# Optimization experiments

Hardware: AMD Instinct MI355X
Metric: run time of the kernel (lower is better)

The kernel has to match this reference:

```python
import jax, jax.numpy as jnp
import numpy as np

B, L, D, H, DF = 8, 1024, 512, 8, 2048
NBLK = 3  # three TemporalAttentionBlocks


def _ln(x, g, b, eps=1e-5):
    m = x.mean(-1, keepdims=True)
    v = x.var(-1, keepdims=True)
    return (x - m) / jnp.sqrt(v + eps) * g + b


def setup_inputs() -> dict:
    key = jax.random.key(0)
    ks = iter(jax.random.split(key, 64))
    def w(i, o):
        return jax.random.normal(next(ks), (i, o), jnp.float32) * (1.0 / np.sqrt(i))
    def ws(n, i, o):
        return jax.random.normal(next(ks), (n, i, o), jnp.float32) * (1.0 / np.sqrt(i))
    return dict(
        x=jax.random.normal(next(ks), (B, L, D), jnp.float32),
        # outer multi-head attention (AttentionLayer) params
        aw_q=w(D, D), ab_q=jnp.zeros((D,), jnp.float32),
        aw_k=w(D, D), ab_k=jnp.zeros((D,), jnp.float32),
        aw_v=w(D, D), ab_v=jnp.zeros((D,), jnp.float32),
        aw_o=w(D, D), ab_o=jnp.zeros((D,), jnp.float32),
        n1g=jnp.ones((D,), jnp.float32), n1b=jnp.zeros((D,), jnp.float32),
        n2g=jnp.ones((D,), jnp.float32), n2b=jnp.zeros((D,), jnp.float32),
        # 3 stacked TemporalAttentionBlock params
        tqw=ws(NBLK, D, D), tqb=jnp.zeros((NBLK, D), jnp.float32),
        tkw=ws(NBLK, D, D), tkb=jnp.zeros((NBLK, D), jnp.float32),
        tvw=ws(NBLK, D, D), tvb=jnp.zeros((NBLK, D), jnp.float32),
        tow=ws(NBLK, D, D), tob=jnp.zeros((NBLK, D), jnp.float32),
        tf1w=ws(NBLK, D, DF), tf1b=jnp.zeros((NBLK, DF), jnp.float32),
        tf2w=ws(NBLK, DF, D), tf2b=jnp.zeros((NBLK, D), jnp.float32),
        tng=jnp.ones((NBLK, D), jnp.float32), tnb=jnp.zeros((NBLK, D), jnp.float32),
    )


def _temporal_block(x, qw, qb, kw, kb, vw, vb, ow, ob, f1w, f1b, f2w, f2b, ng, nb):
    b, l, d = x.shape
    q = x @ qw + qb
    k = x @ kw + kb
    v = x @ vw + vb
    # NOTE: no 1/sqrt(d) scaling, as in the original
    probs = jax.nn.softmax(jnp.einsum('bld,bsd->bls', q, k), axis=-1)
    out = jnp.einsum('bls,bsd->bld', probs, v)
    # faithful to original transpose(1,2).contiguous().view(-1, L, D): a
    # memory-reinterpreting reshape of [B,D,L] into [B,L,D]
    out = jnp.swapaxes(out, 1, 2).reshape(b, l, d)
    x = x + (out @ ow + ob)
    res = x
    xn = _ln(x, ng, nb)
    ff = jax.nn.relu(xn @ f1w + f1b) @ f2w + f2b
    return res + ff


def reference(x, aw_q, ab_q, aw_k, ab_k, aw_v, ab_v, aw_o, ab_o,
              n1g, n1b, n2g, n2b,
              tqw, tqb, tkw, tkb, tvw, tvb, tow, tob,
              tf1w, tf1b, tf2w, tf2b, tng, tnb):
    b, l, d = x.shape
    e = d // H
    q = (x @ aw_q + ab_q).reshape(b, l, H, e)
    k = (x @ aw_k + ab_k).reshape(b, l, H, e)
    v = (x @ aw_v + ab_v).reshape(b, l, H, e)
    A = jax.nn.softmax(jnp.einsum('blhe,bshe->bhls', q, k) / np.sqrt(e).astype(np.float32), axis=-1)
    new_x = jnp.einsum('bhls,bshe->blhe', A, v).reshape(b, l, d) @ aw_o + ab_o
    x = _ln(x + new_x, n1g, n1b)
    y = x
    for i in range(NBLK):
        y = _temporal_block(y, tqw[i], tqb[i], tkw[i], tkb[i], tvw[i], tvb[i],
                            tow[i], tob[i], tf1w[i], tf1b[i], tf2w[i], tf2b[i],
                            tng[i], tnb[i])
    return _ln(x + y, n2g, n2b), A
```

## Files before the change

kernel.cpp:

```cpp
#include <hip/hip_runtime.h>

typedef __bf16 bf16;
typedef __bf16 v8bf __attribute__((ext_vector_type(8)));
typedef float  v4f  __attribute__((ext_vector_type(4)));

#define BM 128
#define BN 128
#define BK 32

enum { EPI_STORE = 0, EPI_RELU = 1, EPI_ADD = 2 };

template <int SPLIT, int EPI, typename CT>
__global__ __launch_bounds__(256)
void gemm_bt(const bf16* __restrict__ A, long plA,
             const bf16* __restrict__ Bt, long plB,
             const float* __restrict__ bias, long sBias,
             const bf16* __restrict__ R, long plR,
             CT* __restrict__ C, long plC,
             int M, int N, int K, int lda, int ldb, int ldc,
             long sA, long sB, long sC, long sR,
             int zdiv, long sA2, long sB2, long sC2,
             float scale)
{
    constexpr int NBUF = SPLIT ? 4 : 2;
    __shared__ __attribute__((aligned(16))) bf16 lds[NBUF * BM * BK];
    bf16* const lAh = lds;
    bf16* const lBh = lds + BM * BK;
    bf16* const lAl = SPLIT ? lds + 2 * BM * BK : lds;
    bf16* const lBl = SPLIT ? lds + 3 * BM * BK : lds;

    const int bz = blockIdx.z;
    const int zq = bz / zdiv;
    const int zr = bz - zq * zdiv;
    A  += (long)zq * sA + (long)zr * sA2;
    Bt += (long)zq * sB + (long)zr * sB2;
    C  += (long)zq * sC + (long)zr * sC2;
    const float* bp = bias ? bias + (long)bz * sBias : nullptr;
    const bf16* Rp = (EPI == EPI_ADD) ? (R + (long)zq * sR) : (const bf16*)nullptr;

    const int tn = blockIdx.x * BN;
    const int tm = blockIdx.y * BM;
    const int tid  = threadIdx.x;
    const int wave = tid >> 6;
    const int lane = tid & 63;
    const int wm   = (wave >> 1) * 64;
    const int wn   = (wave & 1) * 64;
    const int quad = lane >> 4;
    const int l16  = lane & 15;

    v4f acc[4][4];
#pragma unroll
    for (int i = 0; i < 4; ++i)
#pragma unroll
        for (int j = 0; j < 4; ++j) {
            v4f z = {0.f, 0.f, 0.f, 0.f};
            acc[i][j] = z;
        }

    const int sr  = lane >> 2;
    const int scl = (lane & 3) * 8;

    for (int k0 = 0; k0 < K; k0 += BK) {
        __syncthreads();
#pragma unroll
        for (int c = 0; c < 2; ++c) {
            const int chunk = wave * 2 + c;
            const int row   = chunk * 16 + sr;
            {
                const bf16* gp = A + (long)(tm + row) * lda + (k0 + scl);
                __builtin_amdgcn_global_load_lds(
                    (const __attribute__((address_space(1))) void*)gp,
                    (__attribute__((address_space(3))) void*)(lAh + chunk * 512),
                    16, 0, 0);
                if (SPLIT)
                    __builtin_amdgcn_global_load_lds(
                        (const __attribute__((address_space(1))) void*)(gp + plA),
                        (__attribute__((address_space(3))) void*)(lAl + chunk * 512),
                        16, 0, 0);
            }
            {
                int gn = tn + row;
                if (gn > N - 1) gn = N - 1;
                const bf16* gp = Bt + (long)gn * ldb + (k0 + scl);
                __builtin_amdgcn_global_load_lds(
                    (const __attribute__((address_space(1))) void*)gp,
                    (__attribute__((address_space(3))) void*)(lBh + chunk * 512),
                    16, 0, 0);
                if (SPLIT)
                    __builtin_amdgcn_global_load_lds(
                        (const __attribute__((address_space(1))) void*)(gp + plB),
                        (__attribute__((address_space(3))) void*)(lBl + chunk * 512),
                        16, 0, 0);
            }
        }
        __syncthreads();

        v8bf ah[4], bh[4];
#pragma unroll
        for (int i = 0; i < 4; ++i) {
            ah[i] = *(const v8bf*)(lAh + (wm + i * 16 + l16) * 32 + quad * 8);
            bh[i] = *(const v8bf*)(lBh + (wn + i * 16 + l16) * 32 + quad * 8);
        }
#pragma unroll
        for (int i = 0; i < 4; ++i)
#pragma unroll
            for (int j = 0; j < 4; ++j)
                acc[i][j] = __builtin_amdgcn_mfma_f32_16x16x32_bf16(
                    ah[i], bh[j], acc[i][j], 0, 0, 0);
        if (SPLIT) {
            {
                v8bf bl[4];
#pragma unroll
                for (int j = 0; j < 4; ++j)
                    bl[j] = *(const v8bf*)(lBl + (wn + j * 16 + l16) * 32 + quad * 8);
#pragma unroll
                for (int i = 0; i < 4; ++i)
#pragma unroll
                    for (int j = 0; j < 4; ++j)
                        acc[i][j] = __builtin_amdgcn_mfma_f32_16x16x32_bf16(
                            ah[i], bl[j], acc[i][j], 0, 0, 0);
            }
            {
                v8bf al[4];
#pragma unroll
                for (int i = 0; i < 4; ++i)
                    al[i] = *(const v8bf*)(lAl + (wm + i * 16 + l16) * 32 + quad * 8);
#pragma unroll
                for (int i = 0; i < 4; ++i)
#pragma unroll
                    for (int j = 0; j < 4; ++j)
                        acc[i][j] = __builtin_amdgcn_mfma_f32_16x16x32_bf16(
                            al[i], bh[j], acc[i][j], 0, 0, 0);
            }
        }
    }

#pragma unroll
    for (int i = 0; i < 4; ++i) {
        const int r0 = tm + wm + i * 16 + quad * 4;
#pragma unroll
        for (int j = 0; j < 4; ++j) {
            const int col = tn + wn + j * 16 + l16;
            if (col < N) {
                const float bv = bp ? bp[col] : 0.f;
#pragma unroll
                for (int r = 0; r < 4; ++r) {
                    const long off = (long)(r0 + r) * ldc + col;
                    float v = acc[i][j][r] * scale + bv;
                    if (EPI == EPI_RELU) v = v > 0.f ? v : 0.f;
                    if (EPI == EPI_ADD)  v += (float)Rp[off] + (float)Rp[off + plR];
                    if constexpr (sizeof(CT) == 4) {
                        C[off] = (CT)v;
                    } else {
                        const bf16 hi = (bf16)v;
                        C[off]       = hi;
                        C[off + plC] = (bf16)(v - (float)hi);
                    }
                }
            }
        }
    }
}

__global__ void detect_dtype(const void* __restrict__ n1g, int* __restrict__ flag)
{
    if (threadIdx.x == 0 && blockIdx.x == 0)
        *flag = (*(const unsigned*)n1g == 0x3F800000u) ? 1 : 0;
}

__global__ __launch_bounds__(256)
void convert_pairs(const void* __restrict__ src, bf16* __restrict__ dst,
                   long plane, int n, const int* __restrict__ flag)
{
    const bool f32 = (*flag != 0);
    const int base = (blockIdx.x * 256 + threadIdx.x) * 8;
#pragma unroll
    for (int i = 0; i < 8; ++i) {
        const int idx = base + i;
        if (idx < n) {
            const float v = f32 ? ((const float*)src)[idx]
                                : (float)((const bf16*)src)[idx];
            const bf16 hi = (bf16)v;
            dst[idx]         = hi;
            dst[idx + plane] = (bf16)(v - (float)hi);
        }
    }
}

struct Seg { const void* src; float* dst; int n; };
struct SegTab { Seg s[17]; };
__global__ __launch_bounds__(256)
void convert_f32(SegTab tab, const int* __restrict__ flag)
{
    const Seg sg = tab.s[blockIdx.z];
    const bool f32 = (*flag != 0);
    const int idx = blockIdx.x * 256 + threadIdx.x;
    if (idx < sg.n)
        sg.dst[idx] = f32 ? ((const float*)sg.src)[idx]
                          : (float)((const bf16*)sg.src)[idx];
}

__global__ __launch_bounds__(256)
void transpose_split(const void* __restrict__ in, bf16* __restrict__ out,
                     int R, int C, const int* __restrict__ flag)
{
    __shared__ float t[32][33];
    const bool f32 = (*flag != 0);
    const long ib = (long)blockIdx.z * R * C;
    bf16* ob = out + (long)blockIdx.z * 2 * R * C;
    const int c0 = blockIdx.x * 32;
    const int r0 = blockIdx.y * 32;
    const int x  = threadIdx.x & 31;
    const int y4 = threadIdx.x >> 5;
#pragma unroll
    for (int i = 0; i < 4; ++i) {
        const int r = y4 * 4 + i;
        const long gi = ib + (long)(r0 + r) * C + c0 + x;
        t[r][x] = f32 ? ((const float*)in)[gi] : (float)((const bf16*)in)[gi];
    }
    __syncthreads();
#pragma unroll
    for (int i = 0; i < 4; ++i) {
        const int oc = y4 * 4 + i;
        const float w = t[x][oc];
        const bf16 hi = (bf16)w;
        const long oo = (long)(c0 + oc) * R + r0 + x;
        ob[oo]             = hi;
        ob[oo + (long)R * C] = (bf16)(w - (float)hi);
    }
}

__global__ __launch_bounds__(256)
void transpose_pair(const bf16* __restrict__ in, bf16* __restrict__ out,
                    int R, int C, long PL, int NB)
{
    __shared__ bf16 t[32][33];
    const int plane = blockIdx.z / NB;
    const int b     = blockIdx.z % NB;
    const long base = (long)plane * PL + (long)b * R * C;
    const int c0 = blockIdx.x * 32;
    const int r0 = blockIdx.y * 32;
    const int x  = threadIdx.x & 31;
    const int y4 = threadIdx.x >> 5;
#pragma unroll
    for (int i = 0; i < 4; ++i) {
        const int r = y4 * 4 + i;
        t[r][x] = in[base + (long)(r0 + r) * C + c0 + x];
    }
    __syncthreads();
#pragma unroll
    for (int i = 0; i < 4; ++i) {
        const int oc = y4 * 4 + i;
        out[base + (long)(c0 + oc) * R + r0 + x] = t[x][oc];
    }
}

__global__ __launch_bounds__(256)
void softmax_rows(const float* __restrict__ in, bf16* __restrict__ probs,
                  long plP, void* __restrict__ aout, long aoff,
                  const int* __restrict__ flag, int L)
{
    const int row  = blockIdx.x * 4 + (threadIdx.x >> 6);
    const int lane = threadIdx.x & 63;
    const bool f32 = aout && (*flag != 0);
    const float* r = in + (long)row * L;
    const int n = L >> 7;
    float ev[16];
    float mx = -3.4e38f;
    for (int t = 0; t < n; ++t) {
        const float2 xx = *(const float2*)(r + t * 128 + lane * 2);
        ev[2 * t]     = xx.x;
        ev[2 * t + 1] = xx.y;
        mx = fmaxf(mx, fmaxf(xx.x, xx.y));
    }
    for (int o = 32; o; o >>= 1) mx = fmaxf(mx, __shfl_xor(mx, o));
    float s = 0.f;
    for (int t = 0; t < 2 * n; ++t) { ev[t] = __expf(ev[t] - mx); s += ev[t]; }
    for (int o = 32; o; o >>= 1) s += __shfl_xor(s, o);
    const float inv = 1.f / s;
    bf16* w = probs + (long)row * L;
    for (int t = 0; t < n; ++t) {
        const int idx = t * 128 + lane * 2;
        const float p0 = ev[2 * t] * inv;
        const float p1 = ev[2 * t + 1] * inv;
        const bf16 h0 = (bf16)p0, h1 = (bf16)p1;
        union { bf16 b[2]; unsigned u; } uh, ul;
        uh.b[0] = h0; uh.b[1] = h1;
        ul.b[0] = (bf16)(p0 - (float)h0); ul.b[1] = (bf16)(p1 - (float)h1);
        *(unsigned*)(w + idx)       = uh.u;
        *(unsigned*)(w + idx + plP) = ul.u;
        if (aout) {
            const long o2 = aoff + (long)row * L + idx;
            if (f32) {
                float2 f; f.x = p0; f.y = p1;
                *(float2*)((float*)aout + o2) = f;
            } else {
                union { bf16 b[2]; unsigned u; } ua;
                ua.b[0] = (bf16)p0; ua.b[1] = (bf16)p1;
                *(unsigned*)((bf16*)aout + o2) = ua.u;
            }
        }
    }
}

template <bool ADD, bool TO_ANY>
__global__ __launch_bounds__(256)
void ln_rows(const bf16* __restrict__ a, const bf16* __restrict__ b2, long PL,
             const float* __restrict__ g, const float* __restrict__ bb,
             bf16* __restrict__ outp, void* __restrict__ out_any,
             const int* __restrict__ flag)
{
    const int row  = blockIdx.x * 4 + (threadIdx.x >> 6);
    const int lane = threadIdx.x & 63;
    const bool f32 = TO_ANY && (*flag != 0);
    const long base = (long)row * 512;
    float v[8];
    float s = 0.f, s2 = 0.f;
#pragma unroll
    for (int t = 0; t < 4; ++t) {
        const long gi = base + t * 128 + lane * 2;
        union { unsigned u; bf16 b[2]; } hh, ll;
        hh.u = *(const unsigned*)(a + gi);
        ll.u = *(const unsigned*)(a + gi + PL);
        float x0 = (float)hh.b[0] + (float)ll.b[0];
        float x1 = (float)hh.b[1] + (float)ll.b[1];
        if (ADD) {
            union { unsigned u; bf16 b[2]; } h2, l2;
            h2.u = *(const unsigned*)(b2 + gi);
            l2.u = *(const unsigned*)(b2 + gi + PL);
            x0 += (float)h2.b[0] + (float)l2.b[0];
            x1 += (float)h2.b[1] + (float)l2.b[1];
        }
        v[2 * t] = x0; v[2 * t + 1] = x1;
        s += x0 + x1; s2 += x0 * x0 + x1 * x1;
    }
    for (int o = 32; o; o >>= 1) { s += __shfl_xor(s, o); s2 += __shfl_xor(s2, o); }
    const float mean = s * (1.f / 512.f);
    const float var  = s2 * (1.f / 512.f) - mean * mean;
    const float rstd = rsqrtf(var + 1e-5f);
#pragma unroll
    for (int t = 0; t < 4; ++t) {
        const int idx = t * 128 + lane * 2;
        const float o0 = (v[2 * t]     - mean) * rstd * g[idx]     + bb[idx];
        const float o1 = (v[2 * t + 1] - mean) * rstd * g[idx + 1] + bb[idx + 1];
        if (TO_ANY) {
            if (f32) {
                float2 f; f.x = o0; f.y = o1;
                *(float2*)((float*)out_any + base + idx) = f;
            } else {
                union { bf16 b[2]; unsigned u; } ua;
                ua.b[0] = (bf16)o0; ua.b[1] = (bf16)o1;
                *(unsigned*)((bf16*)out_any + base + idx) = ua.u;
            }
        } else {
            union { bf16 b[2]; unsigned u; } uh, ul;
            const bf16 h0 = (bf16)o0, h1 = (bf16)o1;
            uh.b[0] = h0; uh.b[1] = h1;
            ul.b[0] = (bf16)(o0 - (float)h0); ul.b[1] = (bf16)(o1 - (float)h1);
            *(unsigned*)(outp + base + idx)      = uh.u;
            *(unsigned*)(outp + base + idx + PL) = ul.u;
        }
    }
}

extern "C" void kernel_launch(void* const* d_in, const int* in_sizes, int n_in,
                              void* d_out, int out_size, void* d_ws, size_t ws_size,
                              hipStream_t stream)
{
    const int B = 8, L = 1024, D = 512, DF = 2048;
    const long BLD = (long)B * L * D;
    const long PLA = BLD;
    const long PLPF = (long)64 * L * L;
    const long PLF = (long)B * L * DF;
    const long WPL = (long)D * D;
    const long FPL = (long)D * DF;

    char* wsb = (char*)d_ws;
    size_t off = 0;
    auto alloc = [&](size_t bytes) -> void* {
        void* p = wsb + off;
        off = (off + bytes + 255) & ~(size_t)255;
        return p;
    };
    int*   flag  = (int*)alloc(256);
    float* abq_f = (float*)alloc(512 * 4);  float* abk_f = (float*)alloc(512 * 4);
    float* abv_f = (float*)alloc(512 * 4);  float* abo_f = (float*)alloc(512 * 4);
    float* n1g_f = (float*)alloc(512 * 4);  float* n1b_f = (float*)alloc(512 * 4);
    float* n2g_f = (float*)alloc(512 * 4);  float* n2b_f = (float*)alloc(512 * 4);
    float* tqb_f = (float*)alloc(1536 * 4); float* tkb_f = (float*)alloc(1536 * 4);
    float* tvb_f = (float*)alloc(1536 * 4); float* tob_f = (float*)alloc(1536 * 4);
    float* tf1b_f = (float*)alloc(6144 * 4); float* tf2b_f = (float*)alloc(1536 * 4);
    float* tng_f = (float*)alloc(1536 * 4); float* tnb_f = (float*)alloc(1536 * 4);
    bf16* awqT  = (bf16*)alloc((size_t)2 * WPL * 2);
    bf16* awkT  = (bf16*)alloc((size_t)2 * WPL * 2);
    bf16* awvT  = (bf16*)alloc((size_t)2 * WPL * 2);
    bf16* awoT  = (bf16*)alloc((size_t)2 * WPL * 2);
    bf16* tqwT  = (bf16*)alloc((size_t)3 * 2 * WPL * 2);
    bf16* tkwT  = (bf16*)alloc((size_t)3 * 2 * WPL * 2);
    bf16* tvwT  = (bf16*)alloc((size_t)3 * 2 * WPL * 2);
    bf16* towT  = (bf16*)alloc((size_t)3 * 2 * WPL * 2);
    bf16* tf1wT = (bf16*)alloc((size_t)3 * 2 * FPL * 2);
    bf16* tf2wT = (bf16*)alloc((size_t)3 * 2 * FPL * 2);
    bf16* x_s    = (bf16*)alloc((size_t)2 * PLA * 2);
    bf16* q      = (bf16*)alloc((size_t)2 * PLA * 2);
    bf16* k      = (bf16*)alloc((size_t)2 * PLA * 2);
    bf16* v      = (bf16*)alloc((size_t)2 * PLA * 2);
    bf16* vT     = (bf16*)alloc((size_t)2 * PLA * 2);
    bf16* x_attn = (bf16*)alloc((size_t)2 * PLA * 2);
    bf16* res    = (bf16*)alloc((size_t)2 * PLA * 2);
    bf16* probs  = (bf16*)alloc((size_t)2 * PLPF * 2);
    char* big    = (char*)alloc(sizeof(float) * (size_t)PLPF);
    float* logits = (float*)big;
    bf16*  ffh    = (bf16*)big;
    bf16* atmp = v;
    bf16* t_re = q;
    bf16* xn   = k;
    bf16* ybuf = x_s;

    const dim3 blk(256);

    detect_dtype<<<dim3(1), dim3(64), 0, stream>>>(d_in[9], flag);
    SegTab tab;
    tab.s[0]  = { d_in[2],  abq_f,  512 };  tab.s[1]  = { d_in[4],  abk_f,  512 };
    tab.s[2]  = { d_in[6],  abv_f,  512 };  tab.s[3]  = { d_in[8],  abo_f,  512 };
    tab.s[4]  = { d_in[9],  n1g_f,  512 };  tab.s[5]  = { d_in[10], n1b_f,  512 };
    tab.s[6]  = { d_in[11], n2g_f,  512 };  tab.s[7]  = { d_in[12], n2b_f,  512 };
    tab.s[8]  = { d_in[14], tqb_f,  1536 }; tab.s[9]  = { d_in[16], tkb_f,  1536 };
    tab.s[10] = { d_in[18], tvb_f,  1536 }; tab.s[11] = { d_in[20], tob_f,  1536 };
    tab.s[12] = { d_in[22], tf1b_f, 6144 }; tab.s[13] = { d_in[24], tf2b_f, 1536 };
    tab.s[14] = { d_in[25], tng_f,  1536 }; tab.s[15] = { d_in[26], tnb_f,  1536 };
    tab.s[16] = { d_in[26], tnb_f,  1536 };
    convert_f32<<<dim3(24, 1, 17), blk, 0, stream>>>(tab, flag);
    convert_pairs<<<dim3(2048), blk, 0, stream>>>(d_in[0], x_s, PLA, (int)BLD, flag);

    transpose_split<<<dim3(16, 16, 1), blk, 0, stream>>>(d_in[1], awqT, D, D, flag);
    transpose_split<<<dim3(16, 16, 1), blk, 0, stream>>>(d_in[3], awkT, D, D, flag);
    transpose_split<<<dim3(16, 16, 1), blk, 0, stream>>>(d_in[5], awvT, D, D, flag);
    transpose_split<<<dim3(16, 16, 1), blk, 0, stream>>>(d_in[7], awoT, D, D, flag);
    transpose_split<<<dim3(16, 16, 3), blk, 0, stream>>>(d_in[13], tqwT, D, D, flag);
    transpose_split<<<dim3(16, 16, 3), blk, 0, stream>>>(d_in[15], tkwT, D, D, flag);
    transpose_split<<<dim3(16, 16, 3), blk, 0, stream>>>(d_in[17], tvwT, D, D, flag);
    transpose_split<<<dim3(16, 16, 3), blk, 0, stream>>>(d_in[19], towT, D, D, flag);
    transpose_split<<<dim3(64, 16, 3), blk, 0, stream>>>(d_in[21], tf1wT, D, DF, flag);
    transpose_split<<<dim3(16, 64, 3), blk, 0, stream>>>(d_in[23], tf2wT, DF, D, flag);

    gemm_bt<1, EPI_STORE, bf16><<<dim3(4, 64, 3), blk, 0, stream>>>(
        x_s, PLA, awqT, WPL, abq_f, 512, nullptr, 0, q, PLA,
        8192, 512, 512, 512, 512, 512,
        0, (long)2 * WPL, (long)2 * PLA, 0, 1, 0, 0, 0, 1.f);
    transpose_pair<<<dim3(16, 32, 16), blk, 0, stream>>>(v, vT, L, D, PLA, 8);

    gemm_bt<1, EPI_STORE, float><<<dim3(8, 8, 64), blk, 0, stream>>>(
        q, PLA, k, PLA, nullptr, 0, nullptr, 0, logits, 0,
        1024, 1024, 64, 512, 512, 1024,
        (long)L * D, (long)L * D, (long)8 * L * L, 0,
        8, 64, 64, (long)L * L, 0.125f);
    softmax_rows<<<dim3(16384), blk, 0, stream>>>(
        logits, probs, PLPF, d_out, BLD, flag, L);
    gemm_bt<1, EPI_STORE, bf16><<<dim3(1, 8, 64), blk, 0, stream>>>(
        probs, PLPF, vT, PLA, nullptr, 0, nullptr, 0, atmp, PLA,
        1024, 64, 1024, 1024, 1024, 512,
        (long)8 * L * L, (long)D * L, (long)L * D, 0,
        8, (long)L * L, (long)64 * L, 64, 1.f);

    gemm_bt<1, EPI_ADD, bf16><<<dim3(4, 64, 1), blk, 0, stream>>>(
        atmp, PLA, awoT, WPL, abo_f, 0, x_s, PLA, res, PLA,
        8192, 512, 512, 512, 512, 512, 0, 0, 0, 0, 1, 0, 0, 0, 1.f);
    ln_rows<false, false><<<dim3(2048), blk, 0, stream>>>(
        res, nullptr, PLA, n1g_f, n1b_f, x_attn, nullptr, flag);

    const bf16* yin = x_attn;
    for (int t = 0; t < 3; ++t) {
        const bf16* owT = towT + (long)t * 2 * WPL;
        const bf16* f1T = tf1wT + (long)t * 2 * FPL;
        const bf16* f2T = tf2wT + (long)t * 2 * FPL;

        gemm_bt<1, EPI_STORE, bf16><<<dim3(4, 64, 3), blk, 0, stream>>>(
            yin, PLA, tqwT + (long)t * 2 * WPL, WPL, tqb_f + t * D, 1536,
            nullptr, 0, q, PLA,
            8192, 512, 512, 512, 512, 512,
            0, (long)6 * WPL, (long)2 * PLA, 0, 1, 0, 0, 0, 1.f);
        transpose_pair<<<dim3(16, 32, 16), blk, 0, stream>>>(v, vT, L, D, PLA, 8);

        gemm_bt<1, EPI_STORE, float><<<dim3(8, 8, 8), blk, 0, stream>>>(
            q, PLA, k, PLA, nullptr, 0, nullptr, 0, logits, 0,
            1024, 1024, 512, 512, 512, 1024,
            (long)L * D, (long)L * D, (long)L * L, 0, 1, 0, 0, 0, 1.f);
        softmax_rows<<<dim3(2048), blk, 0, stream>>>(
            logits, probs, PLPF, nullptr, 0, flag, L);
        gemm_bt<1, EPI_STORE, bf16><<<dim3(4, 8, 8), blk, 0, stream>>>(
            probs, PLPF, vT, PLA, nullptr, 0, nullptr, 0, atmp, PLA,
            1024, 512, 1024, 1024, 1024, 512,
            (long)L * L, (long)D * L, (long)L * D, 0, 1, 0, 0, 0, 1.f);
        transpose_pair<<<dim3(16, 32, 16), blk, 0, stream>>>(atmp, t_re, L, D, PLA, 8);
        gemm_bt<1, EPI_ADD, bf16><<<dim3(4, 64, 1), blk, 0, stream>>>(
            t_re, PLA, owT, WPL, tob_f + t * D, 0, yin, PLA, res, PLA,
            8192, 512, 512, 512, 512, 512, 0, 0, 0, 0, 1, 0, 0, 0, 1.f);
        ln_rows<false, false><<<dim3(2048), blk, 0, stream>>>(
            res, nullptr, PLA, tng_f + t * D, tnb_f + t * D, xn, nullptr, flag);
        gemm_bt<1, EPI_RELU, bf16><<<dim3(16, 64, 1), blk, 0, stream>>>(
            xn, PLA, f1T, FPL, tf1b_f + t * DF, 0, nullptr, 0, ffh, PLF,
            8192, 2048, 512, 512, 512, 2048, 0, 0, 0, 0, 1, 0, 0, 0, 1.f);
        gemm_bt<1, EPI_ADD, bf16><<<dim3(4, 64, 1), blk, 0, stream>>>(
            ffh, PLF, f2T, FPL, tf2b_f + t * D, 0, res, PLA, ybuf, PLA,
            8192, 512, 2048, 2048, 2048, 512, 0, 0, 0, 0, 1, 0, 0, 0, 1.f);
        yin = ybuf;
    }

    ln_rows<true, true><<<dim3(2048), blk, 0, stream>>>(
        x_attn, ybuf, PLA, n2g_f, n2b_f, nullptr, d_out, flag);
}
```

Before: 2.061 ms.

## Double-buffer GEMM LDS tiles with async prefetch and widen softmax vector loads

```diff
diff --git a/kernel.cpp b/kernel.cpp
--- a/kernel.cpp
+++ b/kernel.cpp
@@ -23,11 +23,8 @@
              float scale)
 {
     constexpr int NBUF = SPLIT ? 4 : 2;
-    __shared__ __attribute__((aligned(16))) bf16 lds[NBUF * BM * BK];
-    bf16* const lAh = lds;
-    bf16* const lBh = lds + BM * BK;
-    bf16* const lAl = SPLIT ? lds + 2 * BM * BK : lds;
-    bf16* const lBl = SPLIT ? lds + 3 * BM * BK : lds;
+    constexpr int TILE = BM * BK;
+    __shared__ __attribute__((aligned(16))) bf16 lds[2 * NBUF * TILE];
 
     const int bz = blockIdx.z;
     const int zq = bz / zdiv;
@@ -59,9 +56,10 @@
 
     const int sr  = lane >> 2;
     const int scl = (lane & 3) * 8;
-
-    for (int k0 = 0; k0 < K; k0 += BK) {
-        __syncthreads();
+    const int nT  = K / BK;
+
+    auto stage = [&](int buf, int k0) {
+        bf16* const dst = lds + buf * (NBUF * TILE);
 #pragma unroll
         for (int c = 0; c < 2; ++c) {
             const int chunk = wave * 2 + c;
@@ -70,12 +68,12 @@
                 const bf16* gp = A + (long)(tm + row) * lda + (k0 + scl);
                 __builtin_amdgcn_global_load_lds(
                     (const __attribute__((address_space(1))) void*)gp,
-                    (__attribute__((address_space(3))) void*)(lAh + chunk * 512),
+                    (__attribute__((address_space(3))) void*)(dst + chunk * 512),
                     16, 0, 0);
                 if (SPLIT)
                     __builtin_amdgcn_global_load_lds(
                         (const __attribute__((address_space(1))) void*)(gp + plA),
-                        (__attribute__((address_space(3))) void*)(lAl + chunk * 512),
+                        (__attribute__((address_space(3))) void*)(dst + 2 * TILE + chunk * 512),
                         16, 0, 0);
             }
             {
@@ -84,16 +82,36 @@
                 const bf16* gp = Bt + (long)gn * ldb + (k0 + scl);
                 __builtin_amdgcn_global_load_lds(
                     (const __attribute__((address_space(1))) void*)gp,
-                    (__attribute__((address_space(3))) void*)(lBh + chunk * 512),
+                    (__attribute__((address_space(3))) void*)(dst + TILE + chunk * 512),
                     16, 0, 0);
                 if (SPLIT)
                     __builtin_amdgcn_global_load_lds(
                         (const __attribute__((address_space(1))) void*)(gp + plB),
-                        (__attribute__((address_space(3))) void*)(lBl + chunk * 512),
+                        (__attribute__((address_space(3))) void*)(dst + 3 * TILE + chunk * 512),
                         16, 0, 0);
             }
         }
-        __syncthreads();
+    };
+
+    stage(0, 0);
+
+    for (int t = 0; t < nT; ++t) {
+        const int cur = t & 1;
+        if (t + 1 < nT) {
+            stage(cur ^ 1, (t + 1) * BK);
+            if constexpr (SPLIT != 0)
+                asm volatile("s_waitcnt vmcnt(8)" ::: "memory");
+            else
+                asm volatile("s_waitcnt vmcnt(4)" ::: "memory");
+        } else {
+            asm volatile("s_waitcnt vmcnt(0)" ::: "memory");
+        }
+        __builtin_amdgcn_s_barrier();
+        asm volatile("" ::: "memory");
+
+        const bf16* const lb  = lds + cur * (NBUF * TILE);
+        const bf16* const lAh = lb;
+        const bf16* const lBh = lb + TILE;
 
         v8bf ah[4], bh[4];
 #pragma unroll
@@ -108,6 +126,8 @@
                 acc[i][j] = __builtin_amdgcn_mfma_f32_16x16x32_bf16(
                     ah[i], bh[j], acc[i][j], 0, 0, 0);
         if (SPLIT) {
+            const bf16* const lAl = lb + 2 * TILE;
+            const bf16* const lBl = lb + 3 * TILE;
             {
                 v8bf bl[4];
 #pragma unroll
@@ -133,6 +153,8 @@
                             al[i], bh[j], acc[i][j], 0, 0, 0);
             }
         }
+        __builtin_amdgcn_s_barrier();
+        asm volatile("" ::: "memory");
     }
 
 #pragma unroll
@@ -264,40 +286,45 @@
     const int lane = threadIdx.x & 63;
     const bool f32 = aout && (*flag != 0);
     const float* r = in + (long)row * L;
-    const int n = L >> 7;
+    const int n = L >> 8;
     float ev[16];
     float mx = -3.4e38f;
     for (int t = 0; t < n; ++t) {
-        const float2 xx = *(const float2*)(r + t * 128 + lane * 2);
-        ev[2 * t]     = xx.x;
-        ev[2 * t + 1] = xx.y;
-        mx = fmaxf(mx, fmaxf(xx.x, xx.y));
+        const float4 xx = *(const float4*)(r + t * 256 + lane * 4);
+        ev[4 * t]     = xx.x;
+        ev[4 * t + 1] = xx.y;
+        ev[4 * t + 2] = xx.z;
+        ev[4 * t + 3] = xx.w;
+        mx = fmaxf(mx, fmaxf(fmaxf(xx.x, xx.y), fmaxf(xx.z, xx.w)));
     }
     for (int o = 32; o; o >>= 1) mx = fmaxf(mx, __shfl_xor(mx, o));
     float s = 0.f;
-    for (int t = 0; t < 2 * n; ++t) { ev[t] = __expf(ev[t] - mx); s += ev[t]; }
+    for (int t = 0; t < 4 * n; ++t) { ev[t] = __expf(ev[t] - mx); s += ev[t]; }
     for (int o = 32; o; o >>= 1) s += __shfl_xor(s, o);
     const float inv = 1.f / s;
     bf16* w = probs + (long)row * L;
     for (int t = 0; t < n; ++t) {
-        const int idx = t * 128 + lane * 2;
-        const float p0 = ev[2 * t] * inv;
-        const float p1 = ev[2 * t + 1] * inv;
-        const bf16 h0 = (bf16)p0, h1 = (bf16)p1;
-        union { bf16 b[2]; unsigned u; } uh, ul;
-        uh.b[0] = h0; uh.b[1] = h1;
-        ul.b[0] = (bf16)(p0 - (float)h0); ul.b[1] = (bf16)(p1 - (float)h1);
-        *(unsigned*)(w + idx)       = uh.u;
-        *(unsigned*)(w + idx + plP) = ul.u;
+        const int idx = t * 256 + lane * 4;
+        float p[4];
+        union { bf16 b[4]; uint2 u; } uh, ul, ua;
+#pragma unroll
+        for (int j = 0; j < 4; ++j) {
+            p[j] = ev[4 * t + j] * inv;
+            const bf16 h = (bf16)p[j];
+            uh.b[j] = h;
+            ul.b[j] = (bf16)(p[j] - (float)h);
+        }
+        *(uint2*)(w + idx)       = uh.u;
+        *(uint2*)(w + idx + plP) = ul.u;
         if (aout) {
             const long o2 = aoff + (long)row * L + idx;
             if (f32) {
-                float2 f; f.x = p0; f.y = p1;
-                *(float2*)((float*)aout + o2) = f;
+                float4 f; f.x = p[0]; f.y = p[1]; f.z = p[2]; f.w = p[3];
+                *(float4*)((float*)aout + o2) = f;
             } else {
-                union { bf16 b[2]; unsigned u; } ua;
-                ua.b[0] = (bf16)p0; ua.b[1] = (bf16)p1;
-                *(unsigned*)((bf16*)aout + o2) = ua.u;
+#pragma unroll
+                for (int j = 0; j < 4; ++j) ua.b[j] = (bf16)p[j];
+                *(uint2*)((bf16*)aout + o2) = ua.u;
             }
         }
     }
```

New measurement: 1.816 ms. -11.9%, faster.
